# Performance work log

Measured on AMD Instinct MI355X. Metric: run time of the kernel, lower is better.

The kernel has to match this reference:

```python
import jax, jax.numpy as jnp
import numpy as np

IN_F = 4096
OUT_F = 4096
RANK = 16
N_BITS = 4
ALPHA = 1.0
GROUP = 128
Q_N = -(2 ** (N_BITS - 1))       # -8 for 4-bit signed
Q_P = 2 ** (N_BITS - 1) - 1      # +7
EPS = 1e-9


def setup_inputs() -> dict:
    key = jax.random.key(0)
    k0, k1, k2, k3, k4, k5 = jax.random.split(key, 6)
    x = jax.random.normal(k0, (8, 1024, IN_F), dtype=jnp.float32)
    w0 = jax.random.normal(k1, (OUT_F, IN_F), dtype=jnp.float32) * 0.02
    lora_a = jax.random.normal(k2, (RANK, IN_F), dtype=jnp.float32) * 0.02
    lora_b = jax.random.normal(k3, (OUT_F, RANK), dtype=jnp.float32) * 0.02
    num_groups = (OUT_F * IN_F) // GROUP
    q_scale = jnp.abs(jax.random.normal(k4, (num_groups,), dtype=jnp.float32)) * 0.01 + 0.005
    bias = jax.random.normal(k5, (OUT_F,), dtype=jnp.float32) * 0.01
    return {"x": x, "w0": w0, "lora_a": lora_a, "lora_b": lora_b,
            "q_scale": q_scale, "bias": bias}


def _quantize_weight(w0, lora_a, lora_b, q_scale):
    # LoRA merge: w_comb = w0 + alpha * (B @ A)   -> (OUT_F, IN_F)
    w_comb = w0 + ALPHA * (lora_b @ lora_a)
    num_groups = w_comb.size // GROUP
    w_g = w_comb.reshape(num_groups, GROUP)          # grouped view
    s = q_scale[:, None]                             # (G, 1) per-group scale
    w_scaled = w_g / (s + EPS)
    clamped = jnp.clip(w_scaled, Q_N, Q_P)
    q_int = jnp.round(clamped)
    w_q = (q_int * s).reshape(w_comb.shape)          # dequantized fake-quant weight
    return w_q


def reference(x, w0, lora_a, lora_b, q_scale, bias):
    w_q = _quantize_weight(w0, lora_a, lora_b, q_scale)
    # F.linear(x, w_q) + bias : (B, S, IN) @ (IN, OUT)
    return jnp.einsum('bsi,oi->bso', x, w_q) + bias
```

## Files before the change

kernel.cpp:

```cpp
#include <hip/hip_runtime.h>
#include <hip/hip_bf16.h>
#include <stdint.h>
#include <stddef.h>

#define IN_F   4096
#define OUT_F  4096
#define RANK   16
#define GROUP  128
#define M_TOT  8192
#define BM     128
#define BN     128
#define BK     32

typedef __bf16 bf16_t;
typedef __bf16 bf16x4 __attribute__((ext_vector_type(4)));
typedef __bf16 bf16x8 __attribute__((ext_vector_type(8)));
typedef float  f32x4  __attribute__((ext_vector_type(4)));

__device__ static inline void load_lds16(const void* g, void* l) {
  __builtin_amdgcn_global_load_lds(
      (const __attribute__((address_space(1))) unsigned int*)g,
      (__attribute__((address_space(3))) unsigned int*)l,
      16, 0, 0);
}

__global__ void __launch_bounds__(256)
quant_kernel(const float* __restrict__ w0, const float* __restrict__ la,
             const float* __restrict__ lb, const float* __restrict__ qs,
             bf16_t* __restrict__ wq)
{
  const int o = blockIdx.y;
  const int i = blockIdx.x * 1024 + threadIdx.x * 4;

  __shared__ float lbr[RANK];
  if (threadIdx.x < RANK) lbr[threadIdx.x] = lb[o * RANK + threadIdx.x];
  __syncthreads();

  const size_t off = (size_t)o * IN_F + i;
  const float4 w = *(const float4*)(w0 + off);
  float a0 = w.x, a1 = w.y, a2 = w.z, a3 = w.w;
  #pragma unroll
  for (int r = 0; r < RANK; ++r) {
    const float4 av = *(const float4*)(la + (size_t)r * IN_F + i);
    const float bv = lbr[r];
    a0 = fmaf(bv, av.x, a0);
    a1 = fmaf(bv, av.y, a1);
    a2 = fmaf(bv, av.z, a2);
    a3 = fmaf(bv, av.w, a3);
  }
  const float s   = qs[o * (IN_F / GROUP) + (i >> 7)];
  const float inv = 1.0f / (s + 1e-9f);
  const float q0 = rintf(fminf(fmaxf(a0 * inv, -8.0f), 7.0f)) * s;
  const float q1 = rintf(fminf(fmaxf(a1 * inv, -8.0f), 7.0f)) * s;
  const float q2 = rintf(fminf(fmaxf(a2 * inv, -8.0f), 7.0f)) * s;
  const float q3 = rintf(fminf(fmaxf(a3 * inv, -8.0f), 7.0f)) * s;
  bf16x4 v;
  v[0] = (bf16_t)q0; v[1] = (bf16_t)q1; v[2] = (bf16_t)q2; v[3] = (bf16_t)q3;
  *(bf16x4*)(wq + off) = v;
}

__global__ void __launch_bounds__(256)
castx_kernel(const float* __restrict__ x, bf16_t* __restrict__ xb)
{
  const size_t i = ((size_t)blockIdx.x * 256 + threadIdx.x) * 8;
  const float4 a = *(const float4*)(x + i);
  const float4 b = *(const float4*)(x + i + 4);
  bf16x8 v;
  v[0] = (bf16_t)a.x; v[1] = (bf16_t)a.y; v[2] = (bf16_t)a.z; v[3] = (bf16_t)a.w;
  v[4] = (bf16_t)b.x; v[5] = (bf16_t)b.y; v[6] = (bf16_t)b.z; v[7] = (bf16_t)b.w;
  *(bf16x8*)(xb + i) = v;
}

__global__ void __launch_bounds__(256)
gemm_kernel(const bf16_t* __restrict__ A, const bf16_t* __restrict__ Bw,
            const float* __restrict__ bias, float* __restrict__ C)
{
  __shared__ __align__(16) bf16_t lA[BM * BK];
  __shared__ __align__(16) bf16_t lB[BN * BK];

  const int tid  = threadIdx.x;
  const int lane = tid & 63;
  const int lr   = lane & 15;
  const int quad = lane >> 4;
  const int wave = tid >> 6;

  const int m0 = blockIdx.y * BM;
  const int n0 = blockIdx.x * BN;

  const int srow = tid >> 2;
  const int scol = (tid & 3) * 8;

  const bf16_t* gA0 = A  + (size_t)(m0 + srow) * IN_F + scol;
  const bf16_t* gA1 = gA0 + (size_t)64 * IN_F;
  const bf16_t* gB0 = Bw + (size_t)(n0 + srow) * IN_F + scol;
  const bf16_t* gB1 = gB0 + (size_t)64 * IN_F;

  char* dA0 = (char*)lA + tid * 16;
  char* dA1 = (char*)lA + (256 + tid) * 16;
  char* dB0 = (char*)lB + tid * 16;
  char* dB1 = (char*)lB + (256 + tid) * 16;

  const int mb = (wave & 1) * 64;
  const int nb = (wave >> 1) * 64;

  f32x4 acc[4][4];
  #pragma unroll
  for (int i = 0; i < 4; ++i)
    #pragma unroll
    for (int j = 0; j < 4; ++j)
      acc[i][j] = (f32x4){0.f, 0.f, 0.f, 0.f};

  for (int kt = 0; kt < IN_F; kt += BK) {
    load_lds16(gA0 + kt, dA0);
    load_lds16(gA1 + kt, dA1);
    load_lds16(gB0 + kt, dB0);
    load_lds16(gB1 + kt, dB1);
    __syncthreads();

    bf16x8 af[4], bfr[4];
    #pragma unroll
    for (int f = 0; f < 4; ++f)
      af[f]  = *(const bf16x8*)(lA + (mb + f * 16 + lr) * BK + quad * 8);
    #pragma unroll
    for (int f = 0; f < 4; ++f)
      bfr[f] = *(const bf16x8*)(lB + (nb + f * 16 + lr) * BK + quad * 8);

    #pragma unroll
    for (int fm = 0; fm < 4; ++fm)
      #pragma unroll
      for (int fn = 0; fn < 4; ++fn)
        acc[fm][fn] = __builtin_amdgcn_mfma_f32_16x16x32_bf16(
            af[fm], bfr[fn], acc[fm][fn], 0, 0, 0);

    __syncthreads();
  }

  #pragma unroll
  for (int fn = 0; fn < 4; ++fn) {
    const int gn = n0 + nb + fn * 16 + lr;
    const float bv = bias[gn];
    #pragma unroll
    for (int fm = 0; fm < 4; ++fm) {
      const int gm = m0 + mb + fm * 16 + quad * 4;
      #pragma unroll
      for (int r = 0; r < 4; ++r)
        C[(size_t)(gm + r) * OUT_F + gn] = acc[fm][fn][r] + bv;
    }
  }
}

extern "C" void kernel_launch(void* const* d_in, const int* in_sizes, int n_in,
                              void* d_out, int out_size, void* d_ws, size_t ws_size,
                              hipStream_t stream) {
  const float* x    = (const float*)d_in[0];
  const float* w0   = (const float*)d_in[1];
  const float* la   = (const float*)d_in[2];
  const float* lb   = (const float*)d_in[3];
  const float* qs   = (const float*)d_in[4];
  const float* bias = (const float*)d_in[5];
  float* out = (float*)d_out;

  bf16_t* wq = (bf16_t*)d_ws;
  bf16_t* xb = (bf16_t*)((char*)d_ws + (size_t)OUT_F * IN_F * 2);

  quant_kernel<<<dim3(IN_F / 1024, OUT_F), 256, 0, stream>>>(w0, la, lb, qs, wq);
  castx_kernel<<<(M_TOT * IN_F) / (256 * 8), 256, 0, stream>>>(x, xb);
  gemm_kernel<<<dim3(OUT_F / BN, M_TOT / BM), 256, 0, stream>>>(xb, wq, bias, out);
}
```

Baseline: 608.6 us.

## Double-buffer LDS tiles in GEMM to overlap global loads with MFMA

The GEMM now keeps two LDS buffers for the A and B tiles. It issues the global-to-LDS loads for the next K tile before computing on the current one, and drops the second barrier per iteration. This aims to hide global memory latency behind the MFMA work. It also adds a launch-bounds hint for three blocks per CU. The cost is twice the LDS per block and a register cap that could cause spills or lower occupancy.

```diff
diff --git a/kernel.cpp b/kernel.cpp
--- a/kernel.cpp
+++ b/kernel.cpp
@@ -11,6 +11,7 @@
 #define BM     128
 #define BN     128
 #define BK     32
+#define NIT    (IN_F / BK)
 
 typedef __bf16 bf16_t;
 typedef __bf16 bf16x4 __attribute__((ext_vector_type(4)));
@@ -71,12 +72,12 @@
   *(bf16x8*)(xb + i) = v;
 }
 
-__global__ void __launch_bounds__(256)
+__global__ void __launch_bounds__(256, 3)
 gemm_kernel(const bf16_t* __restrict__ A, const bf16_t* __restrict__ Bw,
             const float* __restrict__ bias, float* __restrict__ C)
 {
-  __shared__ __align__(16) bf16_t lA[BM * BK];
-  __shared__ __align__(16) bf16_t lB[BN * BK];
+  __shared__ __align__(16) bf16_t lA[2][BM * BK];
+  __shared__ __align__(16) bf16_t lB[2][BN * BK];
 
   const int tid  = threadIdx.x;
   const int lane = tid & 63;
@@ -95,11 +96,6 @@
   const bf16_t* gB0 = Bw + (size_t)(n0 + srow) * IN_F + scol;
   const bf16_t* gB1 = gB0 + (size_t)64 * IN_F;
 
-  char* dA0 = (char*)lA + tid * 16;
-  char* dA1 = (char*)lA + (256 + tid) * 16;
-  char* dB0 = (char*)lB + tid * 16;
-  char* dB1 = (char*)lB + (256 + tid) * 16;
-
   const int mb = (wave & 1) * 64;
   const int nb = (wave >> 1) * 64;
 
@@ -110,20 +106,38 @@
     for (int j = 0; j < 4; ++j)
       acc[i][j] = (f32x4){0.f, 0.f, 0.f, 0.f};
 
-  for (int kt = 0; kt < IN_F; kt += BK) {
-    load_lds16(gA0 + kt, dA0);
-    load_lds16(gA1 + kt, dA1);
-    load_lds16(gB0 + kt, dB0);
-    load_lds16(gB1 + kt, dB1);
+  {
+    char* dA = (char*)lA[0] + tid * 16;
+    char* dB = (char*)lB[0] + tid * 16;
+    load_lds16(gA0, dA);
+    load_lds16(gA1, dA + 4096);
+    load_lds16(gB0, dB);
+    load_lds16(gB1, dB + 4096);
+  }
+
+  int buf = 0;
+  for (int it = 0; it < NIT; ++it) {
     __syncthreads();
 
+    if (it + 1 < NIT) {
+      const int kt = (it + 1) * BK;
+      char* dA = (char*)lA[buf ^ 1] + tid * 16;
+      char* dB = (char*)lB[buf ^ 1] + tid * 16;
+      load_lds16(gA0 + kt, dA);
+      load_lds16(gA1 + kt, dA + 4096);
+      load_lds16(gB0 + kt, dB);
+      load_lds16(gB1 + kt, dB + 4096);
+    }
+
+    const bf16_t* sA = lA[buf];
+    const bf16_t* sB = lB[buf];
     bf16x8 af[4], bfr[4];
     #pragma unroll
     for (int f = 0; f < 4; ++f)
-      af[f]  = *(const bf16x8*)(lA + (mb + f * 16 + lr) * BK + quad * 8);
+      af[f]  = *(const bf16x8*)(sA + (mb + f * 16 + lr) * BK + quad * 8);
     #pragma unroll
     for (int f = 0; f < 4; ++f)
-      bfr[f] = *(const bf16x8*)(lB + (nb + f * 16 + lr) * BK + quad * 8);
+      bfr[f] = *(const bf16x8*)(sB + (nb + f * 16 + lr) * BK + quad * 8);
 
     #pragma unroll
     for (int fm = 0; fm < 4; ++fm)
@@ -132,7 +146,7 @@
         acc[fm][fn] = __builtin_amdgcn_mfma_f32_16x16x32_bf16(
             af[fm], bfr[fn], acc[fm][fn], 0, 0, 0);
 
-    __syncthreads();
+    buf ^= 1;
   }
 
   #pragma unroll
```

Result: no change. 604.0 us (-0.7%).
